# Kernel tuning notes

Measured on AMD Instinct MI355X. Metric: run time of the kernel, lower is better.

The kernel has to match this reference:

```python
import jax, jax.numpy as jnp
import numpy as np

N, E, D, L = 50000, 600000, 128, 3
EPS = 1e-5


def _layer_norm(x, g, b):
    m = jnp.mean(x, axis=-1, keepdims=True)
    v = jnp.mean((x - m) ** 2, axis=-1, keepdims=True)
    return (x - m) * jax.lax.rsqrt(v + EPS) * g + b


def setup_inputs() -> dict:
    key = jax.random.key(0)
    ks = jax.random.split(key, 20)
    s = 1.0 / np.sqrt(D)
    inp = {
        "node": jax.random.normal(ks[0], (N, D), jnp.float32),
        "edge_attr": jax.random.uniform(ks[1], (E,), jnp.float32),
        # stacked per-layer parameters [L, ...]
        "W_rel": jax.random.uniform(ks[2], (L, D, D), jnp.float32, -s, s),
        "b_rel": jax.random.uniform(ks[3], (L, D), jnp.float32, -s, s),
        "W_root": jax.random.uniform(ks[4], (L, D, D), jnp.float32, -s, s),
        "ln1_g": jnp.ones((L, D), jnp.float32),
        "ln1_b": jnp.zeros((L, D), jnp.float32),
        "ln2_g": jnp.ones((L, D), jnp.float32),
        "ln2_b": jnp.zeros((L, D), jnp.float32),
        "W1": jax.random.uniform(ks[5], (L, D, D), jnp.float32, -s, s),
        "b1": jax.random.uniform(ks[6], (L, D), jnp.float32, -s, s),
        "W2": jax.random.uniform(ks[7], (L, D, D), jnp.float32, -s, s),
        "b2": jax.random.uniform(ks[8], (L, D), jnp.float32, -s, s),
        "jk_W": jax.random.uniform(ks[9], (L * D, D), jnp.float32, -1.0 / np.sqrt(L * D), 1.0 / np.sqrt(L * D)),
        "jk_b": jax.random.uniform(ks[10], (D,), jnp.float32, -1.0 / np.sqrt(L * D), 1.0 / np.sqrt(L * D)),
        "edge_index": jax.random.randint(ks[11], (2, E), 0, N, jnp.int64),
        "batch_ptr": jnp.sort(jax.random.randint(ks[12], (51,), 0, N, jnp.int64)),
    }
    return inp


def reference(node, edge_attr, W_rel, b_rel, W_root, ln1_g, ln1_b, ln2_g, ln2_b,
              W1, b1, W2, b2, jk_W, jk_b, edge_index, batch_ptr):
    src, dst = edge_index[0], edge_index[1]
    deg = jax.ops.segment_sum(jnp.ones((E,), node.dtype), dst, num_segments=N)
    inv_deg = 1.0 / jnp.maximum(deg, 1.0)  # nodes with no in-edges -> 0 aggregate
    outs = []
    for l in range(L):
        msg = node[src] * edge_attr[:, None]                       # [E, D] gather
        agg = jax.ops.segment_sum(msg, dst, num_segments=N)        # scatter-sum
        mean = agg * inv_deg[:, None]                              # mean aggregation
        # GraphConv: lin_rel(aggr) + lin_root(x); skip_connection=False
        node = mean @ W_rel[l] + b_rel[l] + node @ W_root[l]
        node = jax.nn.relu(_layer_norm(node @ W1[l] + b1[l], ln1_g[l], ln1_b[l]))
        node = jax.nn.relu(_layer_norm(node @ W2[l] + b2[l], ln2_g[l], ln2_b[l]))
        outs.append(node)
    jk = jnp.concatenate(outs, axis=-1)                            # [N, L*D]
    return jk @ jk_W + jk_b
```

## Files before the change

kernel.cpp:

```cpp
#include <hip/hip_runtime.h>

#define NN 50000
#define EE 600000
#define DD 128
#define CAP 64
#define SLDS_STRIDE 66
#define BINS 196
#define NP (BINS * 256)
#define BINCAP 3584
#define BCSTRIDE 16
#define LDS_STRIDE 136
#define P1_EDGES 2048
#define P1_BLOCKS ((EE + P1_EDGES - 1) / P1_EDGES)

typedef __attribute__((ext_vector_type(8))) short bf16x8;
typedef __attribute__((ext_vector_type(4))) float f32x4;

__device__ __forceinline__ unsigned short f2bf(float f) {
    union { float f; unsigned u; } v; v.f = f;
    unsigned r = v.u + 0x7FFF + ((v.u >> 16) & 1);
    return (unsigned short)(r >> 16);
}
__device__ __forceinline__ float bflo(unsigned x) { return __uint_as_float(x << 16); }
__device__ __forceinline__ float bfhi(unsigned x) { return __uint_as_float(x & 0xffff0000u); }

__global__ __launch_bounds__(256) void fill_p1(
    const int* __restrict__ src, const int* __restrict__ dst, const float* __restrict__ ea,
    int* __restrict__ binCnt, unsigned long long* __restrict__ recs) {
    __shared__ int hist[BINS];
    __shared__ int lstart[BINS];
    __shared__ int gbase[BINS];
    __shared__ int scan[256];
    __shared__ unsigned long long srt[P1_EDGES];
    const int t = threadIdx.x;
    for (int i = t; i < BINS; i += 256) hist[i] = 0;
    __syncthreads();

    unsigned long long rec[8];
    int bin[8], rnk[8];
    bool val[8];
#pragma unroll
    for (int g = 0; g < 2; ++g) {
        int e0 = blockIdx.x * P1_EDGES + g * 1024 + t * 4;
        int4 dv, sv; float4 ev;
        if (e0 + 3 < EE) {
            dv = *(const int4*)&dst[e0];
            sv = *(const int4*)&src[e0];
            ev = *(const float4*)&ea[e0];
        } else {
            int* dp = (int*)&dv; int* sp = (int*)&sv; float* ep = (float*)&ev;
#pragma unroll
            for (int k = 0; k < 4; ++k) {
                int e = e0 + k;
                dp[k] = (e < EE) ? dst[e] : 0;
                sp[k] = (e < EE) ? src[e] : 0;
                ep[k] = (e < EE) ? ea[e] : 0.f;
            }
        }
#pragma unroll
        for (int k = 0; k < 4; ++k) {
            int i = g * 4 + k;
            int e = e0 + k;
            val[i] = (e < EE);
            int d = ((const int*)&dv)[k];
            unsigned w16 = (unsigned)__float2int_rn(((const float*)&ev)[k] * 65535.0f);
            if (w16 > 65535u) w16 = 65535u;
            rec[i] = ((unsigned long long)(unsigned)d << 32) |
                     (((unsigned)((const int*)&sv)[k]) << 16) | w16;
            bin[i] = d >> 8;
            rnk[i] = val[i] ? atomicAdd(&hist[bin[i]], 1) : 0;
        }
    }
    __syncthreads();
    scan[t] = (t < BINS) ? hist[t] : 0;
    __syncthreads();
#pragma unroll
    for (int off = 1; off < 256; off <<= 1) {
        int v = (t >= off) ? scan[t - off] : 0;
        __syncthreads();
        scan[t] += v;
        __syncthreads();
    }
    if (t < BINS) {
        lstart[t] = scan[t] - hist[t];
        gbase[t] = hist[t] ? atomicAdd(&binCnt[t * BCSTRIDE], hist[t]) : 0;
    }
    __syncthreads();
#pragma unroll
    for (int i = 0; i < 8; ++i)
        if (val[i]) srt[lstart[bin[i]] + rnk[i]] = rec[i];
    __syncthreads();
    const int total = scan[255];
    for (int j = t; j < total; j += 256) {
        unsigned long long r = srt[j];
        int b = (int)(r >> 40);
        int o = gbase[b] + (j - lstart[b]);
        if (o < BINCAP) recs[(size_t)b * BINCAP + o] = r;
    }
}

__global__ __launch_bounds__(256) void fill_p2(
    const int* __restrict__ binCnt, const unsigned long long* __restrict__ recs,
    int* __restrict__ cnt, unsigned* __restrict__ slots) {
    __shared__ int cl[128];
    __shared__ unsigned sl[128 * CAP];
    const int b = blockIdx.x >> 1, half = blockIdx.x & 1, t = threadIdx.x;
    if (t < 128) cl[t] = 0;
    __syncthreads();
    int n = binCnt[b * BCSTRIDE];
    if (n > BINCAP) n = BINCAP;
    const unsigned long long* rp = recs + (size_t)b * BINCAP;
    for (int j = t; j < n; j += 256) {
        unsigned long long r = rp[j];
        int dl = (int)(r >> 32) & 255;
        if ((dl >> 7) == half) {
            int p = atomicAdd(&cl[dl & 127], 1);
            if (p < CAP) sl[(dl & 127) * CAP + p] = (unsigned)r;
        }
    }
    __syncthreads();
    const int node0 = (b << 8) + (half << 7);
    if (t < 128) cnt[node0 + t] = cl[t];
    const uint4* s4 = (const uint4*)sl;
    uint4* g4 = (uint4*)(slots + (size_t)node0 * CAP);
    for (int i = t; i < 2048; i += 256) g4[i] = s4[i];
}

#define CONV_BLKS 6250
__global__ void prep_kernel(const float* __restrict__ nodef, unsigned short* __restrict__ node_bf,
                            const float* __restrict__ W_rel, const float* __restrict__ W_root,
                            const float* __restrict__ W1, const float* __restrict__ W2,
                            const float* __restrict__ jkW,
                            const float* __restrict__ b_rel, const float* __restrict__ b1,
                            float* __restrict__ bc, unsigned short* __restrict__ packed,
                            int* __restrict__ binCnt) {
    int b = blockIdx.x;
    if (b < 96) {
        int tg = b * 256 + threadIdx.x;
        int chunk = tg >> 11, r = tg & 2047;
        int lane = r & 63, tile = r >> 6;
        int kt = tile >> 3, nt = tile & 7;
        int quad = lane >> 4, n = lane & 15;
        int k0 = kt * 32 + quad * 8;
        int col = nt * 16 + n;
        union { unsigned short u[8]; uint4 v; } tmp;
        if (chunk < 6) {
            int l = (chunk < 3) ? chunk : chunk - 3;
            const float* A = ((chunk < 3) ? W_rel : W_root) + (size_t)l * 16384;
            const float* B = W1 + (size_t)l * 16384;
            float acc[8] = {0.f, 0.f, 0.f, 0.f, 0.f, 0.f, 0.f, 0.f};
            for (int k = 0; k < 128; ++k) {
                float bv = B[k * 128 + col];
#pragma unroll
                for (int j = 0; j < 8; ++j) acc[j] = fmaf(A[(k0 + j) * 128 + k], bv, acc[j]);
            }
#pragma unroll
            for (int j = 0; j < 8; ++j) tmp.u[j] = f2bf(acc[j]);
        } else {
            const float* s = (chunk < 9) ? (W2 + (size_t)(chunk - 6) * 16384)
                                         : (jkW + (size_t)(chunk - 9) * 16384);
#pragma unroll
            for (int j = 0; j < 8; ++j) tmp.u[j] = f2bf(s[(size_t)(k0 + j) * DD + col]);
        }
        *(uint4*)&packed[(size_t)tg * 8] = tmp.v;
    } else if (b == 96) {
        if (threadIdx.x < BINS) binCnt[threadIdx.x * BCSTRIDE] = 0;
        for (int o = threadIdx.x; o < 384; o += 256) {
            int l = o >> 7, j = o & 127;
            float s = 0.f;
            for (int k = 0; k < 128; ++k)
                s = fmaf(b_rel[l * 128 + k], W1[(size_t)l * 16384 + k * 128 + j], s);
            bc[o] = s + b1[o];
        }
    } else {
        int i = (b - 97) * 256 + threadIdx.x;
        float4 v = *(const float4*)&nodef[(size_t)i * 4];
        ushort4 o;
        o.x = f2bf(v.x); o.y = f2bf(v.y); o.z = f2bf(v.z); o.w = f2bf(v.w);
        *(ushort4*)&node_bf[(size_t)i * 4] = o;
    }
}

template <bool JK>
__global__ __launch_bounds__(64, 4) void fused_layer(
    const unsigned short* __restrict__ feat,
    const unsigned* __restrict__ slots, const int* __restrict__ cnt,
    const unsigned short* __restrict__ PWrel, const unsigned short* __restrict__ PWroot,
    const unsigned short* __restrict__ PW2,
    const float* __restrict__ bc, const float* __restrict__ ln1g, const float* __restrict__ ln1b,
    const float* __restrict__ b2, const float* __restrict__ ln2g, const float* __restrict__ ln2b,
    unsigned short* __restrict__ out,
    const unsigned short* __restrict__ o0, const unsigned short* __restrict__ o1,
    const unsigned short* __restrict__ PJ0, const unsigned short* __restrict__ PJ1,
    const unsigned short* __restrict__ PJ2,
    const float* __restrict__ jkb, float* __restrict__ fout) {
    __shared__ __align__(16) unsigned short wt[16 * LDS_STRIDE];
    __shared__ __align__(16) unsigned slds[16 * SLDS_STRIDE];
    const int lane = threadIdx.x;
    const int mrow = blockIdx.x * 16;
    const int quad = lane >> 4, n15 = lane & 15;
    const int kq   = quad * 8;
    const int i8   = n15 * 8;
    const float wscale = 1.0f / 65535.0f;

    const int cl0 = cnt[mrow + n15];
    const int cAll = (cl0 > CAP) ? CAP : cl0;

    {
        const unsigned* sbase = slots + (size_t)mrow * CAP;
#pragma unroll
        for (int k = 0; k < 4; ++k) {
            int li = k * 64 + lane;
            uint4 v = *(const uint4*)&sbase[li * 4];
            int rw = li >> 4, cu = (li & 15) * 4;
            *(uint4*)&slds[rw * SLDS_STRIDE + cu] = v;
        }
    }

    const unsigned short* An = feat + (size_t)(mrow + n15) * DD;
    bf16x8 an4[4];
#pragma unroll
    for (int kt = 0; kt < 4; ++kt) an4[kt] = *(const bf16x8*)&An[kt * 32 + kq];

    __asm__ __volatile__("s_waitcnt lgkmcnt(0)" ::: "memory");

#pragma unroll
    for (int r = 0; r < 4; ++r) {
        const int row = r * 4 + quad;
        int c = __shfl(cAll, row);
        float acc[8] = {0.f, 0.f, 0.f, 0.f, 0.f, 0.f, 0.f, 0.f};
        for (int j0 = 0; j0 < c; j0 += 4) {
            uint4 sv = *(const uint4*)&slds[row * SLDS_STRIDE + j0];
            unsigned se[4] = {sv.x, sv.y, sv.z, sv.w};
#pragma unroll
            for (int tt = 0; tt < 4; ++tt) {
                bool ok = (j0 + tt) < c;
                unsigned e = se[tt];
                int   srcn = ok ? (int)(e >> 16) : 0;
                float w    = ok ? (float)(e & 0xffffu) * wscale : 0.0f;
                uint4 v = *(const uint4*)&feat[(size_t)srcn * DD + i8];
                acc[0] = fmaf(bflo(v.x), w, acc[0]);
                acc[1] = fmaf(bfhi(v.x), w, acc[1]);
                acc[2] = fmaf(bflo(v.y), w, acc[2]);
                acc[3] = fmaf(bfhi(v.y), w, acc[3]);
                acc[4] = fmaf(bflo(v.z), w, acc[4]);
                acc[5] = fmaf(bfhi(v.z), w, acc[5]);
                acc[6] = fmaf(bflo(v.w), w, acc[6]);
                acc[7] = fmaf(bfhi(v.w), w, acc[7]);
            }
        }
        float id = 1.0f / fmaxf((float)c, 1.0f);
        union { unsigned short u[8]; uint4 v; } o;
#pragma unroll
        for (int k = 0; k < 8; ++k) o.u[k] = f2bf(acc[k] * id);
        *(uint4*)&wt[row * LDS_STRIDE + i8] = o.v;
    }
    __asm__ __volatile__("s_waitcnt lgkmcnt(0)" ::: "memory");

    f32x4 acc[8];
#pragma unroll
    for (int nt = 0; nt < 8; ++nt) acc[nt] = (f32x4){0.f, 0.f, 0.f, 0.f};
#pragma unroll
    for (int kt = 0; kt < 4; ++kt) {
        bf16x8 am = *(const bf16x8*)&wt[n15 * LDS_STRIDE + kt * 32 + kq];
#pragma unroll
        for (int nt = 0; nt < 8; ++nt) {
            bf16x8 brel = *(const bf16x8*)&PWrel[(size_t)((kt * 8 + nt) * 64 + lane) * 8];
            acc[nt] = __builtin_amdgcn_mfma_f32_16x16x32_bf16(am, brel, acc[nt], 0, 0, 0);
            bf16x8 brt = *(const bf16x8*)&PWroot[(size_t)((kt * 8 + nt) * 64 + lane) * 8];
            acc[nt] = __builtin_amdgcn_mfma_f32_16x16x32_bf16(an4[kt], brt, acc[nt], 0, 0, 0);
        }
    }

    float x[8][4];
#pragma unroll
    for (int nt = 0; nt < 8; ++nt) {
        float bv = bc[nt * 16 + n15];
#pragma unroll
        for (int r = 0; r < 4; ++r) x[nt][r] = acc[nt][r] + bv;
    }
    {
        float s[4] = {0, 0, 0, 0}, q[4] = {0, 0, 0, 0};
#pragma unroll
        for (int nt = 0; nt < 8; ++nt)
#pragma unroll
            for (int r = 0; r < 4; ++r) { s[r] += x[nt][r]; q[r] += x[nt][r] * x[nt][r]; }
#pragma unroll
        for (int m = 1; m <= 8; m <<= 1)
#pragma unroll
            for (int r = 0; r < 4; ++r) { s[r] += __shfl_xor(s[r], m); q[r] += __shfl_xor(q[r], m); }
        const float inv = 1.0f / 128.0f;
#pragma unroll
        for (int r = 0; r < 4; ++r) {
            float mu = s[r] * inv;
            float rs = rsqrtf(fmaxf(q[r] * inv - mu * mu, 0.0f) + 1e-5f);
#pragma unroll
            for (int nt = 0; nt < 8; ++nt) {
                float g = ln1g[nt * 16 + n15], bb = ln1b[nt * 16 + n15];
                x[nt][r] = fmaxf((x[nt][r] - mu) * rs * g + bb, 0.0f);
            }
        }
    }

#pragma unroll
    for (int nt = 0; nt < 8; ++nt)
#pragma unroll
        for (int r = 0; r < 4; ++r)
            wt[(quad * 4 + r) * LDS_STRIDE + nt * 16 + n15] = f2bf(x[nt][r]);
    __asm__ __volatile__("s_waitcnt lgkmcnt(0)" ::: "memory");

    f32x4 acc2[8];
#pragma unroll
    for (int nt = 0; nt < 8; ++nt) acc2[nt] = (f32x4){0.f, 0.f, 0.f, 0.f};
#pragma unroll
    for (int kt = 0; kt < 4; ++kt) {
        bf16x8 ah = *(const bf16x8*)&wt[n15 * LDS_STRIDE + kt * 32 + kq];
#pragma unroll
        for (int nt = 0; nt < 8; ++nt) {
            bf16x8 bw = *(const bf16x8*)&PW2[(size_t)((kt * 8 + nt) * 64 + lane) * 8];
            acc2[nt] = __builtin_amdgcn_mfma_f32_16x16x32_bf16(ah, bw, acc2[nt], 0, 0, 0);
        }
    }
#pragma unroll
    for (int nt = 0; nt < 8; ++nt) {
        float bv = b2[nt * 16 + n15];
#pragma unroll
        for (int r = 0; r < 4; ++r) x[nt][r] = acc2[nt][r] + bv;
    }
    {
        float s[4] = {0, 0, 0, 0}, q[4] = {0, 0, 0, 0};
#pragma unroll
        for (int nt = 0; nt < 8; ++nt)
#pragma unroll
            for (int r = 0; r < 4; ++r) { s[r] += x[nt][r]; q[r] += x[nt][r] * x[nt][r]; }
#pragma unroll
        for (int m = 1; m <= 8; m <<= 1)
#pragma unroll
            for (int r = 0; r < 4; ++r) { s[r] += __shfl_xor(s[r], m); q[r] += __shfl_xor(q[r], m); }
        const float inv = 1.0f / 128.0f;
#pragma unroll
        for (int r = 0; r < 4; ++r) {
            float mu = s[r] * inv;
            float rs = rsqrtf(fmaxf(q[r] * inv - mu * mu, 0.0f) + 1e-5f);
#pragma unroll
            for (int nt = 0; nt < 8; ++nt) {
                float g = ln2g[nt * 16 + n15], bb = ln2b[nt * 16 + n15];
                x[nt][r] = fmaxf((x[nt][r] - mu) * rs * g + bb, 0.0f);
            }
        }
    }

    __asm__ __volatile__("s_waitcnt lgkmcnt(0)" ::: "memory");
#pragma unroll
    for (int nt = 0; nt < 8; ++nt)
#pragma unroll
        for (int r = 0; r < 4; ++r)
            wt[(quad * 4 + r) * LDS_STRIDE + nt * 16 + n15] = f2bf(x[nt][r]);
    __asm__ __volatile__("s_waitcnt lgkmcnt(0)" ::: "memory");

    if constexpr (!JK) {
#pragma unroll
        for (int i = 0; i < 4; ++i) {
            int s = i * 512 + lane * 8;
            int r = s >> 7, col = s & 127;
            uint4 v = *(const uint4*)&wt[r * LDS_STRIDE + col];
            *(uint4*)&out[(size_t)(mrow + r) * DD + col] = v;
        }
    } else {
        f32x4 accJ[8];
#pragma unroll
        for (int nt = 0; nt < 8; ++nt) accJ[nt] = (f32x4){0.f, 0.f, 0.f, 0.f};
#pragma unroll
        for (int kt = 0; kt < 4; ++kt) {
            bf16x8 ah = *(const bf16x8*)&wt[n15 * LDS_STRIDE + kt * 32 + kq];
#pragma unroll
            for (int nt = 0; nt < 8; ++nt) {
                bf16x8 bw = *(const bf16x8*)&PJ2[(size_t)((kt * 8 + nt) * 64 + lane) * 8];
                accJ[nt] = __builtin_amdgcn_mfma_f32_16x16x32_bf16(ah, bw, accJ[nt], 0, 0, 0);
            }
        }
        const unsigned short* A0 = o0 + (size_t)(mrow + n15) * DD;
        const unsigned short* A1 = o1 + (size_t)(mrow + n15) * DD;
#pragma unroll
        for (int kt = 0; kt < 4; ++kt) {
            bf16x8 a0 = *(const bf16x8*)&A0[kt * 32 + kq];
            bf16x8 a1 = *(const bf16x8*)&A1[kt * 32 + kq];
#pragma unroll
            for (int nt = 0; nt < 8; ++nt) {
                bf16x8 b0 = *(const bf16x8*)&PJ0[(size_t)((kt * 8 + nt) * 64 + lane) * 8];
                accJ[nt] = __builtin_amdgcn_mfma_f32_16x16x32_bf16(a0, b0, accJ[nt], 0, 0, 0);
                bf16x8 b1 = *(const bf16x8*)&PJ1[(size_t)((kt * 8 + nt) * 64 + lane) * 8];
                accJ[nt] = __builtin_amdgcn_mfma_f32_16x16x32_bf16(a1, b1, accJ[nt], 0, 0, 0);
            }
        }
#pragma unroll
        for (int nt = 0; nt < 8; ++nt) {
            float bv = jkb[nt * 16 + n15];
#pragma unroll
            for (int r = 0; r < 4; ++r)
                fout[(size_t)(mrow + quad * 4 + r) * DD + nt * 16 + n15] = accJ[nt][r] + bv;
        }
    }
}

extern "C" void kernel_launch(void* const* d_in, const int* in_sizes, int n_in,
                              void* d_out, int out_size, void* d_ws, size_t ws_size,
                              hipStream_t stream) {
    const float* node   = (const float*)d_in[0];
    const float* ea     = (const float*)d_in[1];
    const float* W_rel  = (const float*)d_in[2];
    const float* b_rel  = (const float*)d_in[3];
    const float* W_root = (const float*)d_in[4];
    const float* ln1_g  = (const float*)d_in[5];
    const float* ln1_b  = (const float*)d_in[6];
    const float* ln2_g  = (const float*)d_in[7];
    const float* ln2_b  = (const float*)d_in[8];
    const float* W1     = (const float*)d_in[9];
    const float* b1     = (const float*)d_in[10];
    const float* W2     = (const float*)d_in[11];
    const float* b2     = (const float*)d_in[12];
    const float* jk_W   = (const float*)d_in[13];
    const float* jk_b   = (const float*)d_in[14];
    const int*   ei     = (const int*)d_in[15];
    const int* srcI = ei;
    const int* dstI = ei + EE;

    char* ws = (char*)d_ws;
    size_t off = 0;
    auto alloc = [&](size_t bytes) {
        void* p = ws + off;
        off += (bytes + 255) & ~(size_t)255;
        return p;
    };
    int*                binCnt  = (int*)alloc((size_t)BINS * BCSTRIDE * 4);
    unsigned long long* recs    = (unsigned long long*)alloc((size_t)BINS * BINCAP * 8);
    int*                cnt     = (int*)alloc((size_t)NP * 4);
    unsigned*           slots   = (unsigned*)alloc((size_t)NP * CAP * 4);
    unsigned short*     node_bf = (unsigned short*)alloc((size_t)NN * DD * 2);
    unsigned short* outs_bf[2];
    for (int l = 0; l < 2; ++l) outs_bf[l] = (unsigned short*)alloc((size_t)NN * DD * 2);
    float*              bc      = (float*)alloc((size_t)3 * 128 * 4);
    unsigned short*     packed  = (unsigned short*)alloc((size_t)12 * 16384 * 2);

    prep_kernel<<<97 + CONV_BLKS, 256, 0, stream>>>(
        node, node_bf, W_rel, W_root, W1, W2, jk_W, b_rel, b1, bc, packed, binCnt);
    fill_p1<<<P1_BLOCKS, 256, 0, stream>>>(srcI, dstI, ea, binCnt, recs);
    fill_p2<<<BINS * 2, 256, 0, stream>>>(binCnt, recs, cnt, slots);

    const int gblocks = NN / 16;
    unsigned short* cur = node_bf;
    for (int l = 0; l < 3; ++l) {
        if (l < 2) {
            fused_layer<false><<<gblocks, 64, 0, stream>>>(
                cur, slots, cnt,
                packed + (size_t)l * 16384, packed + (size_t)(3 + l) * 16384,
                packed + (size_t)(6 + l) * 16384,
                bc + (size_t)l * DD, ln1_g + (size_t)l * DD, ln1_b + (size_t)l * DD,
                b2 + (size_t)l * DD, ln2_g + (size_t)l * DD, ln2_b + (size_t)l * DD,
                outs_bf[l],
                nullptr, nullptr, nullptr, nullptr, nullptr, nullptr, nullptr);
            cur = outs_bf[l];
        } else {
            fused_layer<true><<<gblocks, 64, 0, stream>>>(
                cur, slots, cnt,
                packed + (size_t)l * 16384, packed + (size_t)(3 + l) * 16384,
                packed + (size_t)(6 + l) * 16384,
                bc + (size_t)l * DD, ln1_g + (size_t)l * DD, ln1_b + (size_t)l * DD,
                b2 + (size_t)l * DD, ln2_g + (size_t)l * DD, ln2_b + (size_t)l * DD,
                nullptr,
                outs_bf[0], outs_bf[1],
                packed + (size_t)9 * 16384, packed + (size_t)10 * 16384, packed + (size_t)11 * 16384,
                jk_b, (float*)d_out);
        }
    }
}
```

Baseline: 258.8 us.

## Merge prep and edge-binning pass into one launch, add MFMA priority hints

The weight-packing/bf16-conversion prep kernel and the first edge-binning pass now run as one kernel with disjoint block ranges. The binCnt zeroing moves to a hipMemsetAsync so the binning blocks no longer depend on the prep blocks. This removes a launch and lets the two independent phases overlap on the device. It also wraps the MFMA loops in the fused layer kernel with s_setprio raise/lower, so matrix waves get issue priority over memory-bound waves. The cost is a larger-LDS combined kernel whose prep blocks now reserve the binning kernel's shared memory, which may reduce occupancy for those blocks.

Result: faster. 248.7 us, median of 2 (-3.9%).

```diff
diff --git a/kernel.cpp b/kernel.cpp
--- a/kernel.cpp
+++ b/kernel.cpp
@@ -12,6 +12,8 @@
 #define LDS_STRIDE 136
 #define P1_EDGES 2048
 #define P1_BLOCKS ((EE + P1_EDGES - 1) / P1_EDGES)
+#define CONV_BLKS 6250
+#define PREP_BLKS (97 + CONV_BLKS)
 
 typedef __attribute__((ext_vector_type(8))) short bf16x8;
 typedef __attribute__((ext_vector_type(4))) float f32x4;
@@ -24,7 +26,13 @@
 __device__ __forceinline__ float bflo(unsigned x) { return __uint_as_float(x << 16); }
 __device__ __forceinline__ float bfhi(unsigned x) { return __uint_as_float(x & 0xffff0000u); }
 
-__global__ __launch_bounds__(256) void fill_p1(
+__global__ __launch_bounds__(256) void prep_fill(
+    const float* __restrict__ nodef, unsigned short* __restrict__ node_bf,
+    const float* __restrict__ W_rel, const float* __restrict__ W_root,
+    const float* __restrict__ W1, const float* __restrict__ W2,
+    const float* __restrict__ jkW,
+    const float* __restrict__ b_rel, const float* __restrict__ b1,
+    float* __restrict__ bc, unsigned short* __restrict__ packed,
     const int* __restrict__ src, const int* __restrict__ dst, const float* __restrict__ ea,
     int* __restrict__ binCnt, unsigned long long* __restrict__ recs) {
     __shared__ int hist[BINS];
@@ -32,111 +40,11 @@
     __shared__ int gbase[BINS];
     __shared__ int scan[256];
     __shared__ unsigned long long srt[P1_EDGES];
+    const int b = blockIdx.x;
     const int t = threadIdx.x;
-    for (int i = t; i < BINS; i += 256) hist[i] = 0;
-    __syncthreads();
-
-    unsigned long long rec[8];
-    int bin[8], rnk[8];
-    bool val[8];
-#pragma unroll
-    for (int g = 0; g < 2; ++g) {
-        int e0 = blockIdx.x * P1_EDGES + g * 1024 + t * 4;
-        int4 dv, sv; float4 ev;
-        if (e0 + 3 < EE) {
-            dv = *(const int4*)&dst[e0];
-            sv = *(const int4*)&src[e0];
-            ev = *(const float4*)&ea[e0];
-        } else {
-            int* dp = (int*)&dv; int* sp = (int*)&sv; float* ep = (float*)&ev;
-#pragma unroll
-            for (int k = 0; k < 4; ++k) {
-                int e = e0 + k;
-                dp[k] = (e < EE) ? dst[e] : 0;
-                sp[k] = (e < EE) ? src[e] : 0;
-                ep[k] = (e < EE) ? ea[e] : 0.f;
-            }
-        }
-#pragma unroll
-        for (int k = 0; k < 4; ++k) {
-            int i = g * 4 + k;
-            int e = e0 + k;
-            val[i] = (e < EE);
-            int d = ((const int*)&dv)[k];
-            unsigned w16 = (unsigned)__float2int_rn(((const float*)&ev)[k] * 65535.0f);
-            if (w16 > 65535u) w16 = 65535u;
-            rec[i] = ((unsigned long long)(unsigned)d << 32) |
-                     (((unsigned)((const int*)&sv)[k]) << 16) | w16;
-            bin[i] = d >> 8;
-            rnk[i] = val[i] ? atomicAdd(&hist[bin[i]], 1) : 0;
-        }
-    }
-    __syncthreads();
-    scan[t] = (t < BINS) ? hist[t] : 0;
-    __syncthreads();
-#pragma unroll
-    for (int off = 1; off < 256; off <<= 1) {
-        int v = (t >= off) ? scan[t - off] : 0;
-        __syncthreads();
-        scan[t] += v;
-        __syncthreads();
-    }
-    if (t < BINS) {
-        lstart[t] = scan[t] - hist[t];
-        gbase[t] = hist[t] ? atomicAdd(&binCnt[t * BCSTRIDE], hist[t]) : 0;
-    }
-    __syncthreads();
-#pragma unroll
-    for (int i = 0; i < 8; ++i)
-        if (val[i]) srt[lstart[bin[i]] + rnk[i]] = rec[i];
-    __syncthreads();
-    const int total = scan[255];
-    for (int j = t; j < total; j += 256) {
-        unsigned long long r = srt[j];
-        int b = (int)(r >> 40);
-        int o = gbase[b] + (j - lstart[b]);
-        if (o < BINCAP) recs[(size_t)b * BINCAP + o] = r;
-    }
-}
-
-__global__ __launch_bounds__(256) void fill_p2(
-    const int* __restrict__ binCnt, const unsigned long long* __restrict__ recs,
-    int* __restrict__ cnt, unsigned* __restrict__ slots) {
-    __shared__ int cl[128];
-    __shared__ unsigned sl[128 * CAP];
-    const int b = blockIdx.x >> 1, half = blockIdx.x & 1, t = threadIdx.x;
-    if (t < 128) cl[t] = 0;
-    __syncthreads();
-    int n = binCnt[b * BCSTRIDE];
-    if (n > BINCAP) n = BINCAP;
-    const unsigned long long* rp = recs + (size_t)b * BINCAP;
-    for (int j = t; j < n; j += 256) {
-        unsigned long long r = rp[j];
-        int dl = (int)(r >> 32) & 255;
-        if ((dl >> 7) == half) {
-            int p = atomicAdd(&cl[dl & 127], 1);
-            if (p < CAP) sl[(dl & 127) * CAP + p] = (unsigned)r;
-        }
-    }
-    __syncthreads();
-    const int node0 = (b << 8) + (half << 7);
-    if (t < 128) cnt[node0 + t] = cl[t];
-    const uint4* s4 = (const uint4*)sl;
-    uint4* g4 = (uint4*)(slots + (size_t)node0 * CAP);
-    for (int i = t; i < 2048; i += 256) g4[i] = s4[i];
-}
-
-#define CONV_BLKS 6250
-__global__ void prep_kernel(const float* __restrict__ nodef, unsigned short* __restrict__ node_bf,
-                            const float* __restrict__ W_rel, const float* __restrict__ W_root,
-                            const float* __restrict__ W1, const float* __restrict__ W2,
-                            const float* __restrict__ jkW,
-                            const float* __restrict__ b_rel, const float* __restrict__ b1,
-                            float* __restrict__ bc, unsigned short* __restrict__ packed,
-                            int* __restrict__ binCnt) {
-    int b = blockIdx.x;
+
     if (b < 96) {
-        int tg = b * 256 + threadIdx.x;
+        int tg = b * 256 + t;
         int chunk = tg >> 11, r = tg & 2047;
         int lane = r & 63, tile = r >> 6;
         int kt = tile >> 3, nt = tile & 7;
@@ -163,22 +71,117 @@
             for (int j = 0; j < 8; ++j) tmp.u[j] = f2bf(s[(size_t)(k0 + j) * DD + col]);
         }
         *(uint4*)&packed[(size_t)tg * 8] = tmp.v;
+        return;
     } else if (b == 96) {
-        if (threadIdx.x < BINS) binCnt[threadIdx.x * BCSTRIDE] = 0;
-        for (int o = threadIdx.x; o < 384; o += 256) {
+        for (int o = t; o < 384; o += 256) {
             int l = o >> 7, j = o & 127;
             float s = 0.f;
             for (int k = 0; k < 128; ++k)
                 s = fmaf(b_rel[l * 128 + k], W1[(size_t)l * 16384 + k * 128 + j], s);
             bc[o] = s + b1[o];
         }
-    } else {
-        int i = (b - 97) * 256 + threadIdx.x;
+        return;
+    } else if (b < PREP_BLKS) {
+        int i = (b - 97) * 256 + t;
         float4 v = *(const float4*)&nodef[(size_t)i * 4];
         ushort4 o;
         o.x = f2bf(v.x); o.y = f2bf(v.y); o.z = f2bf(v.z); o.w = f2bf(v.w);
         *(ushort4*)&node_bf[(size_t)i * 4] = o;
-    }
+        return;
+    }
+
+    const int pb = b - PREP_BLKS;
+    for (int i = t; i < BINS; i += 256) hist[i] = 0;
+    __syncthreads();
+
+    unsigned long long rec[8];
+    int bin[8], rnk[8];
+    bool val[8];
+#pragma unroll
+    for (int g = 0; g < 2; ++g) {
+        int e0 = pb * P1_EDGES + g * 1024 + t * 4;
+        int4 dv, sv; float4 ev;
+        if (e0 + 3 < EE) {
+            dv = *(const int4*)&dst[e0];
+            sv = *(const int4*)&src[e0];
+            ev = *(const float4*)&ea[e0];
+        } else {
+            int* dp = (int*)&dv; int* sp = (int*)&sv; float* ep = (float*)&ev;
+#pragma unroll
+            for (int k = 0; k < 4; ++k) {
+                int e = e0 + k;
+                dp[k] = (e < EE) ? dst[e] : 0;
+                sp[k] = (e < EE) ? src[e] : 0;
+                ep[k] = (e < EE) ? ea[e] : 0.f;
+            }
+        }
+#pragma unroll
+        for (int k = 0; k < 4; ++k) {
+            int i = g * 4 + k;
+            int e = e0 + k;
+            val[i] = (e < EE);
+            int d = ((const int*)&dv)[k];
+            unsigned w16 = (unsigned)__float2int_rn(((const float*)&ev)[k] * 65535.0f);
+            if (w16 > 65535u) w16 = 65535u;
+            rec[i] = ((unsigned long long)(unsigned)d << 32) |
+                     (((unsigned)((const int*)&sv)[k]) << 16) | w16;
+            bin[i] = d >> 8;
+            rnk[i] = val[i] ? atomicAdd(&hist[bin[i]], 1) : 0;
+        }
+    }
+    __syncthreads();
+    scan[t] = (t < BINS) ? hist[t] : 0;
+    __syncthreads();
+#pragma unroll
+    for (int off = 1; off < 256; off <<= 1) {
+        int v = (t >= off) ? scan[t - off] : 0;
+        __syncthreads();
+        scan[t] += v;
+        __syncthreads();
+    }
+    if (t < BINS) {
+        lstart[t] = scan[t] - hist[t];
+        gbase[t] = hist[t] ? atomicAdd(&binCnt[t * BCSTRIDE], hist[t]) : 0;
+    }
+    __syncthreads();
+#pragma unroll
+    for (int i = 0; i < 8; ++i)
+        if (val[i]) srt[lstart[bin[i]] + rnk[i]] = rec[i];
+    __syncthreads();
+    const int total = scan[255];
+    for (int j = t; j < total; j += 256) {
+        unsigned long long r = srt[j];
+        int bb = (int)(r >> 40);
+        int o = gbase[bb] + (j - lstart[bb]);
+        if (o < BINCAP) recs[(size_t)bb * BINCAP + o] = r;
+    }
+}
+
+__global__ __launch_bounds__(256) void fill_p2(
+    const int* __restrict__ binCnt, const unsigned long long* __restrict__ recs,
+    int* __restrict__ cnt, unsigned* __restrict__ slots) {
+    __shared__ int cl[128];
+    __shared__ unsigned sl[128 * CAP];
+    const int b = blockIdx.x >> 1, half = blockIdx.x & 1, t = threadIdx.x;
+    if (t < 128) cl[t] = 0;
+    __syncthreads();
+    int n = binCnt[b * BCSTRIDE];
+    if (n > BINCAP) n = BINCAP;
+    const unsigned long long* rp = recs + (size_t)b * BINCAP;
+    for (int j = t; j < n; j += 256) {
+        unsigned long long r = rp[j];
+        int dl = (int)(r >> 32) & 255;
+        if ((dl >> 7) == half) {
+            int p = atomicAdd(&cl[dl & 127], 1);
+            if (p < CAP) sl[(dl & 127) * CAP + p] = (unsigned)r;
+        }
+    }
+    __syncthreads();
+    const int node0 = (b << 8) + (half << 7);
+    if (t < 128) cnt[node0 + t] = cl[t];
+    const uint4* s4 = (const uint4*)sl;
+    uint4* g4 = (uint4*)(slots + (size_t)node0 * CAP);
+    for (int i = t; i < 2048; i += 256) g4[i] = s4[i];
 }
 
 template <bool JK>
@@ -260,6 +263,7 @@
     f32x4 acc[8];
 #pragma unroll
     for (int nt = 0; nt < 8; ++nt) acc[nt] = (f32x4){0.f, 0.f, 0.f, 0.f};
+    __builtin_amdgcn_s_setprio(1);
 #pragma unroll
     for (int kt = 0; kt < 4; ++kt) {
         bf16x8 am = *(const bf16x8*)&wt[n15 * LDS_STRIDE + kt * 32 + kq];
@@ -271,6 +275,7 @@
             acc[nt] = __builtin_amdgcn_mfma_f32_16x16x32_bf16(an4[kt], brt, acc[nt], 0, 0, 0);
         }
     }
+    __builtin_amdgcn_s_setprio(0);
 
     float x[8][4];
 #pragma unroll
@@ -312,6 +317,7 @@
     f32x4 acc2[8];
 #pragma unroll
     for (int nt = 0; nt < 8; ++nt) acc2[nt] = (f32x4){0.f, 0.f, 0.f, 0.f};
+    __builtin_amdgcn_s_setprio(1);
 #pragma unroll
     for (int kt = 0; kt < 4; ++kt) {
         bf16x8 ah = *(const bf16x8*)&wt[n15 * LDS_STRIDE + kt * 32 + kq];
@@ -321,6 +327,7 @@
             acc2[nt] = __builtin_amdgcn_mfma_f32_16x16x32_bf16(ah, bw, acc2[nt], 0, 0, 0);
         }
     }
+    __builtin_amdgcn_s_setprio(0);
 #pragma unroll
     for (int nt = 0; nt < 8; ++nt) {
         float bv = b2[nt * 16 + n15];
@@ -370,6 +377,7 @@
         f32x4 accJ[8];
 #pragma unroll
         for (int nt = 0; nt < 8; ++nt) accJ[nt] = (f32x4){0.f, 0.f, 0.f, 0.f};
+        __builtin_amdgcn_s_setprio(1);
 #pragma unroll
         for (int kt = 0; kt < 4; ++kt) {
             bf16x8 ah = *(const bf16x8*)&wt[n15 * LDS_STRIDE + kt * 32 + kq];
@@ -393,6 +401,7 @@
                 accJ[nt] = __builtin_amdgcn_mfma_f32_16x16x32_bf16(a1, b1, accJ[nt], 0, 0, 0);
             }
         }
+        __builtin_amdgcn_s_setprio(0);
 #pragma unroll
         for (int nt = 0; nt < 8; ++nt) {
             float bv = jkb[nt * 16 + n15];
@@ -442,9 +451,10 @@
     float*              bc      = (float*)alloc((size_t)3 * 128 * 4);
     unsigned short*     packed  = (unsigned short*)alloc((size_t)12 * 16384 * 2);
 
-    prep_kernel<<<97 + CONV_BLKS, 256, 0, stream>>>(
-        node, node_bf, W_rel, W_root, W1, W2, jk_W, b_rel, b1, bc, packed, binCnt);
-    fill_p1<<<P1_BLOCKS, 256, 0, stream>>>(srcI, dstI, ea, binCnt, recs);
+    hipMemsetAsync(binCnt, 0, (size_t)BINS * BCSTRIDE * 4, stream);
+    prep_fill<<<PREP_BLKS + P1_BLOCKS, 256, 0, stream>>>(
+        node, node_bf, W_rel, W_root, W1, W2, jk_W, b_rel, b1, bc, packed,
+        srcI, dstI, ea, binCnt, recs);
     fill_p2<<<BINS * 2, 256, 0, stream>>>(binCnt, recs, cnt, slots);
 
     const int gblocks = NN / 16;
```
